# Kernel tuning notes

Hardware: AMD Instinct MI355X
Metric: run time of the kernel (lower is better)

The kernel has to match this reference:

```python
import jax, jax.numpy as jnp
import numpy as np

K, D = 512, 256
NUM_CLASSES, SHARED_KEYS = 10, 10
B, H, W = 32, 64, 64
TRAINING = True


def setup_inputs() -> dict:
    key = jax.random.key(0)
    k1, k2, k3 = jax.random.split(key, 3)
    z_e_x = jax.random.normal(k1, (B, D, H, W), dtype=jnp.float32)
    labels = jax.random.randint(k2, (B,), 0, NUM_CLASSES)
    # nn.Embedding weight initialized uniform(-1/K, 1/K)
    codebook = jax.random.uniform(k3, (K, D), minval=-1.0 / K, maxval=1.0 / K,
                                  dtype=jnp.float32)
    return {"z_e_x": z_e_x, "codebook": codebook, "labels": labels}


def _irrelevant_regions(labels_flat, k, num_classes, n_shared, training):
    # uniform partition of the first K - n_shared codes over the classes
    uniform = jnp.round(jnp.linspace(-0.5, num_classes - 0.51, k - n_shared))  # [K-Ns]
    irrel = uniform[None, :] != labels_flat[:, None].astype(uniform.dtype)     # [N, K-Ns]
    n = labels_flat.shape[0]
    if training:
        tail = jnp.ones((n, n_shared), dtype=bool)   # TRAIN: shared keys masked out
    else:
        tail = jnp.zeros((n, n_shared), dtype=bool)
    return jnp.concatenate([irrel, tail], axis=1)    # [N, K]


def reference(z_e_x, codebook, labels):
    x = jnp.transpose(z_e_x, (0, 2, 3, 1))           # [B,H,W,D]
    xf = x.reshape(-1, D)                            # [N,D], N=B*H*W
    labels_flat = jnp.repeat(labels, H * W)          # [N]

    irrel = _irrelevant_regions(labels_flat, K, NUM_CLASSES, SHARED_KEYS, TRAINING)

    cb_sqr = jnp.sum(codebook * codebook, axis=1)                      # [K]
    in_sqr = jnp.sum(xf * xf, axis=1, keepdims=True)                   # [N,1]
    distances = in_sqr + cb_sqr[None, :] - 2.0 * (xf @ codebook.T)     # [N,K]
    distances = jnp.where(irrel, jnp.inf, distances)

    idx = jnp.argmin(distances, axis=1)                                # [N]

    codes = codebook[idx].reshape(x.shape)                             # [B,H,W,D]
    # straight-through path (detached codebook in torch)
    z_q = x + jax.lax.stop_gradient(codes - x)
    z_q_x = jnp.transpose(z_q, (0, 3, 1, 2))                           # [B,D,H,W]
    # non-detached codebook lookup path
    z_q_bar = codebook[jax.lax.stop_gradient(idx)].reshape(x.shape)
    z_q_x_bar = jnp.transpose(z_q_bar, (0, 3, 1, 2))                   # [B,D,H,W]
    return (z_q_x, z_q_x_bar)
```

## Files before the change

### kernel.cpp

```cpp
#include <hip/hip_runtime.h>


#define D       256
#define KCODES  512
#define HW      4096
#define BATCH   32
#define NPTS    (BATCH * HW)
#define WPW     13

__constant__ int c_cls_start[11] = {0, 51, 101, 151, 201, 251, 301, 352, 402, 452, 502};

__global__ __launch_bounds__(256) void prep_kernel(const float* __restrict__ cb,
                                                   float* __restrict__ cbT,
                                                   float* __restrict__ cbs) {
    const int k = blockIdx.x;
    const int d = threadIdx.x;
    float v = cb[k * D + d];
    cbT[(size_t)d * KCODES + k] = v;
    __shared__ double red[256];
    red[d] = (double)v * (double)v;
    __syncthreads();
    for (int s = 128; s > 0; s >>= 1) {
        if (d < s) red[d] += red[d + s];
        __syncthreads();
    }
    if (d == 0) cbs[k] = (float)red[0];
}

__global__ __launch_bounds__(256) void vq_kernel(const float* __restrict__ z,
                                                 const int* __restrict__ labels,
                                                 const float* __restrict__ cbT,
                                                 const float* __restrict__ cbs,
                                                 float* __restrict__ out) {
    const int lane = threadIdx.x & 63;
    const int w    = __builtin_amdgcn_readfirstlane(threadIdx.x >> 6);
    const int b    = blockIdx.x >> 6;
    const int hw   = ((blockIdx.x & 63) << 6) | lane;
    const int lab  = __builtin_amdgcn_readfirstlane(labels[b]);
    const int c0   = c_cls_start[lab];
    const int cnt  = c_cls_start[lab + 1] - c0;
    const int kbase = c0 + w * WPW;
    const int myn   = min(WPW, cnt - w * WPW);

    const float* __restrict__ xp = z + (size_t)b * (D * HW) + hw;

    float acc[WPW];
#pragma unroll
    for (int j = 0; j < WPW; ++j) acc[j] = 0.0f;

    double xsq = 0.0;

    float xb[4];
#pragma unroll
    for (int i = 0; i < 4; ++i) xb[i] = xp[(size_t)i * HW];

    for (int d = 0; d < D; d += 4) {
        float xn[4];
#pragma unroll
        for (int i = 0; i < 4; ++i) {
            int dn = (d + 4 + i) & (D - 1);
            xn[i] = xp[(size_t)dn * HW];
        }
#pragma unroll
        for (int i = 0; i < 4; ++i) {
            const float* __restrict__ wd = cbT + (size_t)(d + i) * KCODES + kbase;
            const float x = xb[i];
            xsq = fma((double)x, (double)x, xsq);
#pragma unroll
            for (int j = 0; j < WPW; ++j)
                acc[j] = fmaf(x, wd[j], acc[j]);
        }
#pragma unroll
        for (int i = 0; i < 4; ++i) xb[i] = xn[i];
    }

    const float insq = (float)xsq;
    float best = __builtin_inff();
    int bi = kbase;
#pragma unroll
    for (int j = 0; j < WPW; ++j) {
        if (j < myn) {
            float T    = insq + cbs[kbase + j];
            float dist = fmaf(-2.0f, acc[j], T);
            if (dist < best) { best = dist; bi = kbase + j; }
        }
    }

    __shared__ float sd[4][64];
    __shared__ int   si[4][64];
    sd[w][lane] = best;
    si[w][lane] = bi;
    __syncthreads();
    float fb = sd[0][lane];
    int   fi = si[0][lane];
#pragma unroll
    for (int w2 = 1; w2 < 4; ++w2) {
        float dv = sd[w2][lane];
        if (dv < fb) { fb = dv; fi = si[w2][lane]; }
    }

    float* __restrict__ o0 = out + (size_t)b * (D * HW) + hw;
    float* __restrict__ o1 = o0 + (size_t)NPTS * D;
    const int d0 = w * 64;
    for (int d = d0; d < d0 + 64; ++d) {
        float v = cbT[(size_t)d * KCODES + fi];
        o0[(size_t)d * HW] = v;
        o1[(size_t)d * HW] = v;
    }
}

extern "C" void kernel_launch(void* const* d_in, const int* in_sizes, int n_in,
                              void* d_out, int out_size, void* d_ws, size_t ws_size,
                              hipStream_t stream) {
    const float* z      = (const float*)d_in[0];
    const float* cb     = (const float*)d_in[1];
    const int*   labels = (const int*)d_in[2];
    float* out = (float*)d_out;

    float* cbT = (float*)d_ws;
    float* cbs = cbT + (size_t)D * KCODES;

    hipLaunchKernelGGL(prep_kernel, dim3(KCODES), dim3(D), 0, stream, cb, cbT, cbs);
    hipLaunchKernelGGL(vq_kernel, dim3(NPTS / 64), dim3(256), 0, stream,
                       z, labels, cbT, cbs, out);
}
```

Baseline: 404.2 us.

## Pack per-class codebook into padded 64-wide layout with float4 loads

Replaces the transposed full codebook with a per-class packed layout padded to 64 codes, so each wave reads 16 contiguous, aligned weights per dimension as four float4 loads instead of 13 unaligned scalar loads. Padding slots get a huge squared norm, which removes the per-code bounds check in the argmin. An inline-asm zero VGPR offset keeps the weight pointer in vector registers, and launch bounds request 8 blocks per SM. In exchange the kernel does more FMAs on padded codes, adds a third small prep kernel, and the wider accumulator array may raise register pressure.

```diff
diff --git a/kernel.cpp b/kernel.cpp
--- a/kernel.cpp
+++ b/kernel.cpp
@@ -6,43 +6,54 @@
 #define HW      4096
 #define BATCH   32
 #define NPTS    (BATCH * HW)
-#define WPW     13
+#define NCLS    10
+#define WPW     16
 
 __constant__ int c_cls_start[11] = {0, 51, 101, 151, 201, 251, 301, 352, 402, 452, 502};
 
-__global__ __launch_bounds__(256) void prep_kernel(const float* __restrict__ cb,
-                                                   float* __restrict__ cbT,
-                                                   float* __restrict__ cbs) {
-    const int k = blockIdx.x;
-    const int d = threadIdx.x;
-    float v = cb[k * D + d];
-    cbT[(size_t)d * KCODES + k] = v;
-    __shared__ double red[256];
-    red[d] = (double)v * (double)v;
-    __syncthreads();
-    for (int s = 128; s > 0; s >>= 1) {
-        if (d < s) red[d] += red[d + s];
-        __syncthreads();
-    }
-    if (d == 0) cbs[k] = (float)red[0];
+__global__ __launch_bounds__(64) void pack_kernel(const float* __restrict__ cb,
+                                                  float* __restrict__ wpk) {
+    const int c = blockIdx.x >> 8;
+    const int d = blockIdx.x & 255;
+    const int j = threadIdx.x;
+    const int c0 = c_cls_start[c], cnt = c_cls_start[c + 1] - c0;
+    float v = 0.0f;
+    if (j < cnt) v = cb[(size_t)(c0 + j) * D + d];
+    wpk[((size_t)c * D + d) * 64 + j] = v;
 }
 
-__global__ __launch_bounds__(256) void vq_kernel(const float* __restrict__ z,
-                                                 const int* __restrict__ labels,
-                                                 const float* __restrict__ cbT,
-                                                 const float* __restrict__ cbs,
-                                                 float* __restrict__ out) {
+__global__ __launch_bounds__(64) void wsq_kernel(const float* __restrict__ cb,
+                                                 float* __restrict__ wsq) {
+    const int c = blockIdx.x;
+    const int j = threadIdx.x;
+    const int c0 = c_cls_start[c], cnt = c_cls_start[c + 1] - c0;
+    float r = 1e30f;
+    if (j < cnt) {
+        const float* __restrict__ row = cb + (size_t)(c0 + j) * D;
+        double s = 0.0;
+        for (int d = 0; d < D; ++d) { double a = (double)row[d]; s = fma(a, a, s); }
+        r = (float)s;
+    }
+    wsq[c * 64 + j] = r;
+}
+
+__global__ __launch_bounds__(256, 8) void vq_kernel(const float* __restrict__ z,
+                                                    const int* __restrict__ labels,
+                                                    const float* __restrict__ wpk,
+                                                    const float* __restrict__ wsq,
+                                                    float* __restrict__ out) {
     const int lane = threadIdx.x & 63;
     const int w    = __builtin_amdgcn_readfirstlane(threadIdx.x >> 6);
     const int b    = blockIdx.x >> 6;
     const int hw   = ((blockIdx.x & 63) << 6) | lane;
     const int lab  = __builtin_amdgcn_readfirstlane(labels[b]);
-    const int c0   = c_cls_start[lab];
-    const int cnt  = c_cls_start[lab + 1] - c0;
-    const int kbase = c0 + w * WPW;
-    const int myn   = min(WPW, cnt - w * WPW);
+
+    int vz;
+    asm volatile("v_mov_b32 %0, 0" : "=v"(vz));
 
     const float* __restrict__ xp = z + (size_t)b * (D * HW) + hw;
+    const float4* __restrict__ wp =
+        (const float4*)(wpk + ((size_t)lab * D) * 64 + (w * WPW) + vz);
 
     float acc[WPW];
 #pragma unroll
@@ -63,27 +74,43 @@
         }
 #pragma unroll
         for (int i = 0; i < 4; ++i) {
-            const float* __restrict__ wd = cbT + (size_t)(d + i) * KCODES + kbase;
+            const float4 w0 = wp[(size_t)(d + i) * 16 + 0];
+            const float4 w1 = wp[(size_t)(d + i) * 16 + 1];
+            const float4 w2 = wp[(size_t)(d + i) * 16 + 2];
+            const float4 w3 = wp[(size_t)(d + i) * 16 + 3];
             const float x = xb[i];
             xsq = fma((double)x, (double)x, xsq);
-#pragma unroll
-            for (int j = 0; j < WPW; ++j)
-                acc[j] = fmaf(x, wd[j], acc[j]);
+            acc[ 0] = fmaf(x, w0.x, acc[ 0]);
+            acc[ 1] = fmaf(x, w0.y, acc[ 1]);
+            acc[ 2] = fmaf(x, w0.z, acc[ 2]);
+            acc[ 3] = fmaf(x, w0.w, acc[ 3]);
+            acc[ 4] = fmaf(x, w1.x, acc[ 4]);
+            acc[ 5] = fmaf(x, w1.y, acc[ 5]);
+            acc[ 6] = fmaf(x, w1.z, acc[ 6]);
+            acc[ 7] = fmaf(x, w1.w, acc[ 7]);
+            acc[ 8] = fmaf(x, w2.x, acc[ 8]);
+            acc[ 9] = fmaf(x, w2.y, acc[ 9]);
+            acc[10] = fmaf(x, w2.z, acc[10]);
+            acc[11] = fmaf(x, w2.w, acc[11]);
+            acc[12] = fmaf(x, w3.x, acc[12]);
+            acc[13] = fmaf(x, w3.y, acc[13]);
+            acc[14] = fmaf(x, w3.z, acc[14]);
+            acc[15] = fmaf(x, w3.w, acc[15]);
         }
 #pragma unroll
         for (int i = 0; i < 4; ++i) xb[i] = xn[i];
     }
 
     const float insq = (float)xsq;
+    const int jbase = w * WPW;
+    const float* __restrict__ wsqc = wsq + lab * 64 + jbase;
     float best = __builtin_inff();
-    int bi = kbase;
+    int bi = jbase;
 #pragma unroll
     for (int j = 0; j < WPW; ++j) {
-        if (j < myn) {
-            float T    = insq + cbs[kbase + j];
-            float dist = fmaf(-2.0f, acc[j], T);
-            if (dist < best) { best = dist; bi = kbase + j; }
-        }
+        float T    = insq + wsqc[j];
+        float dist = fmaf(-2.0f, acc[j], T);
+        if (dist < best) { best = dist; bi = jbase + j; }
     }
 
     __shared__ float sd[4][64];
@@ -101,9 +128,10 @@
 
     float* __restrict__ o0 = out + (size_t)b * (D * HW) + hw;
     float* __restrict__ o1 = o0 + (size_t)NPTS * D;
+    const float* __restrict__ wrb = wpk + ((size_t)lab * D) * 64 + fi;
     const int d0 = w * 64;
     for (int d = d0; d < d0 + 64; ++d) {
-        float v = cbT[(size_t)d * KCODES + fi];
+        float v = wrb[(size_t)d * 64];
         o0[(size_t)d * HW] = v;
         o1[(size_t)d * HW] = v;
     }
@@ -117,10 +145,11 @@
     const int*   labels = (const int*)d_in[2];
     float* out = (float*)d_out;
 
-    float* cbT = (float*)d_ws;
-    float* cbs = cbT + (size_t)D * KCODES;
+    float* wpk = (float*)d_ws;
+    float* wsq = wpk + (size_t)NCLS * D * 64;
 
-    hipLaunchKernelGGL(prep_kernel, dim3(KCODES), dim3(D), 0, stream, cb, cbT, cbs);
+    hipLaunchKernelGGL(pack_kernel, dim3(NCLS * 256), dim3(64), 0, stream, cb, wpk);
+    hipLaunchKernelGGL(wsq_kernel, dim3(NCLS), dim3(64), 0, stream, cb, wsq);
     hipLaunchKernelGGL(vq_kernel, dim3(NPTS / 64), dim3(256), 0, stream,
-                       z, labels, cbT, cbs, out);
+                       z, labels, wpk, wsq, out);
 }
```

Measured after the change: 648.6 us. 1.6x slower.
